# Kernel tuning notes

Hardware: AMD Instinct MI355X
Metric: run time of the kernel (lower is better)

Reference implementation:

```python
import jax, jax.numpy as jnp
import numpy as np

N = 50000   # nodes
E = 800000  # edges
IN, H, C = 256, 128, 4


def _gcn_norm(edge_index, n):
    """Add self-loops and compute symmetric GCN normalization per edge."""
    loops = jnp.arange(n, dtype=edge_index.dtype)
    src = jnp.concatenate([edge_index[0], loops])
    dst = jnp.concatenate([edge_index[1], loops])
    deg = jax.ops.segment_sum(jnp.ones_like(dst, dtype=jnp.float32), dst,
                              num_segments=n)
    dinv = jnp.where(deg > 0, jax.lax.rsqrt(deg), 0.0)
    norm = dinv[src] * dinv[dst]  # [E+N]
    return src, dst, norm


def _gcn_conv(h, src, dst, norm, W, b, n):
    h = h @ W                              # [N, out]
    msg = h[src] * norm[:, None]           # gather + scale, [E+N, out]
    agg = jax.ops.segment_sum(msg, dst, num_segments=n)
    return agg + b


def setup_inputs() -> dict:
    key = jax.random.key(0)
    ks = jax.random.split(key, 5)
    x = jax.random.normal(ks[0], (N, IN), dtype=jnp.float32)
    edge_index = jax.random.randint(ks[1], (2, E), 0, N, dtype=jnp.int32)
    W1 = jax.random.normal(ks[2], (IN, H), dtype=jnp.float32) * (1.0 / np.sqrt(IN))
    b1 = jnp.zeros((H,), dtype=jnp.float32)
    W2 = jax.random.normal(ks[3], (H, C), dtype=jnp.float32) * (1.0 / np.sqrt(H))
    b2 = jnp.zeros((C,), dtype=jnp.float32)
    return {"x": x, "edge_index": edge_index, "W1": W1, "b1": b1,
            "W2": W2, "b2": b2}


def reference(x, edge_index, W1, b1, W2, b2):
    n = x.shape[0]
    src, dst, norm = _gcn_norm(edge_index, n)
    h = jax.nn.relu(_gcn_conv(x, src, dst, norm, W1, b1, n))
    out = _gcn_conv(h, src, dst, norm, W2, b2, n)
    return out
```

## Files before the change

### kernel.cpp

```cpp
#include <hip/hip_runtime.h>
#include <stdint.h>

typedef __attribute__((ext_vector_type(8))) short short8;
typedef __attribute__((ext_vector_type(4))) float f32x4;
typedef __attribute__((ext_vector_type(8))) uint16_t u16x8;

#define EPB 8192
#define BKT_SHIFT 8

static __device__ __forceinline__ uint16_t f_to_bf16(float f) {
  uint32_t u = __float_as_uint(f);
  uint32_t rounding = 0x7fffu + ((u >> 16) & 1u);
  return (uint16_t)((u + rounding) >> 16);
}

__global__ __launch_bounds__(256) void k_bcount(const int* __restrict__ ei, int E,
                                                int* __restrict__ bcnt) {
  __shared__ int hist[256];
  int tid = threadIdx.x;
  hist[tid] = 0;
  __syncthreads();
  int base = blockIdx.x * EPB;
  int nT = min(EPB, E - base);
  for (int i = tid; i < nT; i += 256)
    atomicAdd(&hist[ei[E + base + i] >> BKT_SHIFT], 1);
  __syncthreads();
  int v = hist[tid];
  if (v) atomicAdd(&bcnt[tid], v);
}

__global__ __launch_bounds__(256) void k_bscan(const int* __restrict__ bcnt, int nbkt,
                                               int* __restrict__ bbase,
                                               int* __restrict__ wbase,
                                               int* __restrict__ row_ptr, int n, int E) {
  __shared__ int ws[4];
  int tid = threadIdx.x, lane = tid & 63, wid = tid >> 6;
  int v = (tid < nbkt) ? bcnt[tid] : 0;
  int s = v;
  #pragma unroll
  for (int off = 1; off < 64; off <<= 1) {
    int t2 = __shfl_up(s, off);
    if (lane >= off) s += t2;
  }
  if (lane == 63) ws[wid] = s;
  __syncthreads();
  int add = 0;
  #pragma unroll
  for (int w = 0; w < 4; ++w)
    if (w < wid) add += ws[w];
  int excl = add + s - v;
  if (tid <= nbkt) bbase[tid] = excl;
  if (tid < nbkt) wbase[tid] = excl;
  if (tid == 0) row_ptr[n] = E;
}

__global__ __launch_bounds__(256) void k_bscatter(const int* __restrict__ ei, int E,
                                                  int* __restrict__ wbase,
                                                  uint32_t* __restrict__ coo) {
  __shared__ uint32_t pk[EPB], pko[EPB];
  __shared__ uint8_t bk[EPB], bko[EPB];
  __shared__ int hist[256], hscan[256], gbase[256], cur[256];
  __shared__ int ws[4];
  int tid = threadIdx.x;
  hist[tid] = 0;
  cur[tid] = 0;
  __syncthreads();
  int base = blockIdx.x * EPB;
  int nT = min(EPB, E - base);
  for (int i = tid; i < nT; i += 256) {
    int s = ei[base + i];
    int d = ei[E + base + i];
    int b = d >> BKT_SHIFT;
    pk[i] = ((uint32_t)(d & ((1 << BKT_SHIFT) - 1)) << 16) | (uint32_t)s;
    bk[i] = (uint8_t)b;
    atomicAdd(&hist[b], 1);
  }
  __syncthreads();
  {
    int lane = tid & 63, wid = tid >> 6;
    int v = hist[tid], s = v;
    #pragma unroll
    for (int off = 1; off < 64; off <<= 1) {
      int t2 = __shfl_up(s, off);
      if (lane >= off) s += t2;
    }
    if (lane == 63) ws[wid] = s;
    __syncthreads();
    int add = 0;
    #pragma unroll
    for (int w = 0; w < 4; ++w)
      if (w < wid) add += ws[w];
    hscan[tid] = add + s - v;
    if (v) gbase[tid] = atomicAdd(&wbase[tid], v);
  }
  __syncthreads();
  for (int i = tid; i < nT; i += 256) {
    int b = bk[i];
    int p = hscan[b] + atomicAdd(&cur[b], 1);
    pko[p] = pk[i];
    bko[p] = (uint8_t)b;
  }
  __syncthreads();
  for (int i = tid; i < nT; i += 256) {
    int b = bko[i];
    coo[gbase[b] + (i - hscan[b])] = pko[i];
  }
}

__global__ __launch_bounds__(256) void k_bcsr(const uint32_t* __restrict__ coo,
                                              const int* __restrict__ bbase,
                                              int* __restrict__ row_ptr,
                                              float* __restrict__ dinv,
                                              int* __restrict__ col, int n) {
  __shared__ int hist[256], lscan[256], cur[256];
  __shared__ int ws[4];
  int tid = threadIdx.x, bkt = blockIdx.x;
  int base = bbase[bkt];
  int cnt = bbase[bkt + 1] - base;
  hist[tid] = 0;
  cur[tid] = 0;
  __syncthreads();
  for (int i = tid; i < cnt; i += 256)
    atomicAdd(&hist[coo[base + i] >> 16], 1);
  __syncthreads();
  {
    int lane = tid & 63, wid = tid >> 6;
    int v = hist[tid], s = v;
    #pragma unroll
    for (int off = 1; off < 64; off <<= 1) {
      int t2 = __shfl_up(s, off);
      if (lane >= off) s += t2;
    }
    if (lane == 63) ws[wid] = s;
    __syncthreads();
    int add = 0;
    #pragma unroll
    for (int w = 0; w < 4; ++w)
      if (w < wid) add += ws[w];
    lscan[tid] = add + s - v;
  }
  __syncthreads();
  int v = (bkt << BKT_SHIFT) + tid;
  if (v < n) {
    row_ptr[v] = base + lscan[tid];
    dinv[v] = rsqrtf((float)(hist[tid] + 1));
  }
  for (int i = tid; i < cnt; i += 256) {
    uint32_t p = coo[base + i];
    int local = p >> 16;
    int pos = lscan[local] + atomicAdd(&cur[local], 1);
    col[base + pos] = (int)(p & 0xffffu);
  }
}

__global__ void k_transpose_w1(const float* __restrict__ W1,
                               uint16_t* __restrict__ W1t) {
  int i = blockIdx.x * blockDim.x + threadIdx.x;
  int k = i >> 7, nn = i & 127;
  W1t[nn * 256 + k] = f_to_bf16(W1[i]);
}

__global__ __launch_bounds__(256) void k_gemm1(const float* __restrict__ x,
                                               const uint16_t* __restrict__ W1t,
                                               const float* __restrict__ dinv,
                                               uint16_t* __restrict__ g, int n) {
  constexpr int LDB = 264;
  __shared__ uint16_t bT[128 * LDB];
  int tid = threadIdx.x, lane = tid & 63, wid = tid >> 6;
  int brow = blockIdx.x * 128;

  {
    int row = tid >> 1, half = tid & 1;
    const u16x8* src = (const u16x8*)(W1t + row * 256 + half * 128);
    u16x8* dst = (u16x8*)(bT + row * LDB + half * 128);
    #pragma unroll
    for (int j = 0; j < 16; ++j) dst[j] = src[j];
  }
  __syncthreads();

  f32x4 acc[2][8];
  #pragma unroll
  for (int i = 0; i < 2; ++i)
    #pragma unroll
    for (int j = 0; j < 8; ++j) acc[i][j] = (f32x4)0.0f;

  int r0 = brow + wid * 32 + (lane & 15);
  int r1 = r0 + 16;
  const float* xr0 = x + (size_t)r0 * 256 + (lane >> 4) * 8;
  const float* xr1 = x + (size_t)r1 * 256 + (lane >> 4) * 8;
  bool ok0 = r0 < n, ok1 = r1 < n;

  #pragma unroll 2
  for (int ks = 0; ks < 8; ++ks) {
    f32x4 a0a = ok0 ? *(const f32x4*)(xr0 + ks * 32) : (f32x4)0.0f;
    f32x4 a0b = ok0 ? *(const f32x4*)(xr0 + ks * 32 + 4) : (f32x4)0.0f;
    f32x4 a1a = ok1 ? *(const f32x4*)(xr1 + ks * 32) : (f32x4)0.0f;
    f32x4 a1b = ok1 ? *(const f32x4*)(xr1 + ks * 32 + 4) : (f32x4)0.0f;
    short8 af0, af1;
    #pragma unroll
    for (int j = 0; j < 4; ++j) {
      af0[j] = (short)f_to_bf16(a0a[j]);
      af0[4 + j] = (short)f_to_bf16(a0b[j]);
      af1[j] = (short)f_to_bf16(a1a[j]);
      af1[4 + j] = (short)f_to_bf16(a1b[j]);
    }
    #pragma unroll
    for (int nt = 0; nt < 8; ++nt) {
      short8 bfr = *(const short8*)&bT[(nt * 16 + (lane & 15)) * LDB + ks * 32 + (lane >> 4) * 8];
      acc[0][nt] = __builtin_amdgcn_mfma_f32_16x16x32_bf16(af0, bfr, acc[0][nt], 0, 0, 0);
      acc[1][nt] = __builtin_amdgcn_mfma_f32_16x16x32_bf16(af1, bfr, acc[1][nt], 0, 0, 0);
    }
  }
  #pragma unroll
  for (int rf = 0; rf < 2; ++rf) {
    #pragma unroll
    for (int r = 0; r < 4; ++r) {
      int orow = brow + wid * 32 + rf * 16 + (lane >> 4) * 4 + r;
      if (orow < n) {
        float dv = dinv[orow];
        #pragma unroll
        for (int nt = 0; nt < 8; ++nt) {
          g[(size_t)orow * 128 + nt * 16 + (lane & 15)] = f_to_bf16(acc[rf][nt][r] * dv);
        }
      }
    }
  }
}

__global__ __launch_bounds__(256) void k_agg1(const uint16_t* __restrict__ g,
                                              const int* __restrict__ row_ptr,
                                              const int* __restrict__ col,
                                              const float* __restrict__ dinv,
                                              const float* __restrict__ b1,
                                              const float* __restrict__ W2,
                                              float* __restrict__ g2, int n) {
  int lane = threadIdx.x & 63, wid = threadIdx.x >> 6;
  int v = blockIdx.x * 4 + wid;
  if (v >= n) return;
  const uint32_t* gw = (const uint32_t*)g;
  uint32_t u = gw[(size_t)v * 64 + lane];
  float s0 = __uint_as_float(u << 16);
  float s1 = __uint_as_float(u & 0xffff0000u);
  int beg = row_ptr[v], end = row_ptr[v + 1];
  for (int base = beg; base < end; base += 64) {
    int idx = base + lane;
    int cv = (idx < end) ? col[idx] : v;
    int m = min(64, end - base);
    int nb = (m + 15) >> 4;
    for (int t = 0; t < nb; ++t) {
      int bb = t * 16;
      uint32_t r[16];
      #pragma unroll
      for (int j = 0; j < 16; ++j) {
        int uu = __shfl(cv, bb + j);
        r[j] = gw[(size_t)uu * 64 + lane];
      }
      int mm = m - bb;
      #pragma unroll
      for (int j = 0; j < 16; ++j) {
        if (j < mm) {
          s0 += __uint_as_float(r[j] << 16);
          s1 += __uint_as_float(r[j] & 0xffff0000u);
        }
      }
    }
  }
  float dv = dinv[v];
  float h0 = fmaxf(dv * s0 + b1[2 * lane], 0.0f);
  float h1 = fmaxf(dv * s1 + b1[2 * lane + 1], 0.0f);
  f32x4 w0 = *(const f32x4*)&W2[lane * 8];
  f32x4 w1 = *(const f32x4*)&W2[lane * 8 + 4];
  float p[4];
  #pragma unroll
  for (int c = 0; c < 4; ++c) p[c] = h0 * w0[c] + h1 * w1[c];
  #pragma unroll
  for (int off = 1; off < 64; off <<= 1) {
    #pragma unroll
    for (int c = 0; c < 4; ++c) p[c] += __shfl_xor(p[c], off);
  }
  if (lane == 0) {
    f32x4 o = {dv * p[0], dv * p[1], dv * p[2], dv * p[3]};
    *(f32x4*)&g2[(size_t)v * 4] = o;
  }
}

__global__ void k_agg2(const float* __restrict__ g2, const int* __restrict__ row_ptr,
                       const int* __restrict__ col, const float* __restrict__ dinv,
                       const float* __restrict__ b2, float* __restrict__ out,
                       int n) {
  int v = blockIdx.x * blockDim.x + threadIdx.x;
  if (v >= n) return;
  const f32x4* g4 = (const f32x4*)g2;
  f32x4 a = g4[v];
  int j = row_ptr[v], end = row_ptr[v + 1];
  for (; j + 8 <= end; j += 8) {
    int u[8];
    #pragma unroll
    for (int q = 0; q < 8; ++q) u[q] = col[j + q];
    f32x4 r[8];
    #pragma unroll
    for (int q = 0; q < 8; ++q) r[q] = g4[u[q]];
    a += ((r[0] + r[1]) + (r[2] + r[3])) + ((r[4] + r[5]) + (r[6] + r[7]));
  }
  for (; j < end; ++j) a += g4[col[j]];
  float dv = dinv[v];
  f32x4 o;
  #pragma unroll
  for (int c = 0; c < 4; ++c) o[c] = dv * a[c] + b2[c];
  *(f32x4*)&out[(size_t)v * 4] = o;
}

extern "C" void kernel_launch(void* const* d_in, const int* in_sizes, int n_in,
                              void* d_out, int out_size, void* d_ws, size_t ws_size,
                              hipStream_t stream) {
  const float* x  = (const float*)d_in[0];
  const int* ei   = (const int*)d_in[1];
  const float* W1 = (const float*)d_in[2];
  const float* b1 = (const float*)d_in[3];
  const float* W2 = (const float*)d_in[4];
  const float* b2 = (const float*)d_in[5];
  float* out = (float*)d_out;
  int n = in_sizes[0] / 256;
  int E = in_sizes[1] / 2;
  int nbkt = (n + 255) >> BKT_SHIFT;

  char* ws = (char*)d_ws;
  size_t off = 0;
  auto alloc = [&](size_t bytes) -> void* {
    void* p = (void*)(ws + off);
    off += (bytes + 255) & ~(size_t)255;
    return p;
  };
  int* bcnt     = (int*)alloc((size_t)nbkt * 4);
  int* bbase    = (int*)alloc((size_t)(nbkt + 1) * 4);
  int* wbase    = (int*)alloc((size_t)nbkt * 4);
  uint32_t* coo = (uint32_t*)alloc((size_t)E * 4);
  int* row_ptr  = (int*)alloc((size_t)(n + 1) * 4);
  int* colA     = (int*)alloc((size_t)E * 4);
  float* dinv   = (float*)alloc((size_t)n * 4);
  uint16_t* W1t = (uint16_t*)alloc((size_t)256 * 128 * 2);
  uint16_t* g   = (uint16_t*)alloc((size_t)n * 128 * 2);
  float* g2     = (float*)alloc((size_t)n * 4 * 4);

  int ebk = (E + EPB - 1) / EPB;
  hipMemsetAsync(bcnt, 0, (size_t)nbkt * 4, stream);
  k_bcount<<<dim3(ebk), dim3(256), 0, stream>>>(ei, E, bcnt);
  k_bscan<<<dim3(1), dim3(256), 0, stream>>>(bcnt, nbkt, bbase, wbase, row_ptr, n, E);
  k_bscatter<<<dim3(ebk), dim3(256), 0, stream>>>(ei, E, wbase, coo);
  k_bcsr<<<dim3(nbkt), dim3(256), 0, stream>>>(coo, bbase, row_ptr, dinv, colA, n);
  k_transpose_w1<<<dim3(128), dim3(256), 0, stream>>>(W1, W1t);
  k_gemm1<<<dim3((n + 127) / 128), dim3(256), 0, stream>>>(x, W1t, dinv, g, n);
  k_agg1<<<dim3((n + 3) / 4), dim3(256), 0, stream>>>(g, row_ptr, colA, dinv, b1, W2, g2, n);
  k_agg2<<<dim3((n + 255) / 256), dim3(256), 0, stream>>>(g2, row_ptr, colA, dinv, b2, out, n);
}
```

Measured before the change: 192.9 us.

## Fold bucket scan and W1 prep into neighbouring kernels, prelayout W1 fragments

Result: faster. 186.4 us (-3.4%).

```diff
diff --git a/kernel.cpp b/kernel.cpp
--- a/kernel.cpp
+++ b/kernel.cpp
@@ -1,11 +1,12 @@
 #include <hip/hip_runtime.h>
+#include <hip/hip_bf16.h>
 #include <stdint.h>
 
 typedef __attribute__((ext_vector_type(8))) short short8;
 typedef __attribute__((ext_vector_type(4))) float f32x4;
 typedef __attribute__((ext_vector_type(8))) uint16_t u16x8;
 
-#define EPB 8192
+#define EPB 2048
 #define BKT_SHIFT 8
 
 static __device__ __forceinline__ uint16_t f_to_bf16(float f) {
@@ -13,11 +14,46 @@
   uint32_t rounding = 0x7fffu + ((u >> 16) & 1u);
   return (uint16_t)((u + rounding) >> 16);
 }
-
-__global__ __launch_bounds__(256) void k_bcount(const int* __restrict__ ei, int E,
-                                                int* __restrict__ bcnt) {
+static __device__ __forceinline__ uint32_t pk2_bf16(float a, float b) {
+  float2 f2; f2.x = a; f2.y = b;
+  __hip_bfloat162 h = __float22bfloat162_rn(f2);
+  return *reinterpret_cast<uint32_t*>(&h);
+}
+
+static __device__ __forceinline__ int excl_scan256(int v, int* ws, int tid) {
+  int lane = tid & 63, wid = tid >> 6;
+  int s = v;
+  #pragma unroll
+  for (int off = 1; off < 64; off <<= 1) {
+    int t2 = __shfl_up(s, off);
+    if (lane >= off) s += t2;
+  }
+  if (lane == 63) ws[wid] = s;
+  __syncthreads();
+  int add = 0;
+  #pragma unroll
+  for (int w = 0; w < 4; ++w)
+    if (w < wid) add += ws[w];
+  return add + s - v;
+}
+
+__global__ __launch_bounds__(256) void k_bcount_w1(const int* __restrict__ ei, int E,
+                                                   int ebk, int* __restrict__ bcnt,
+                                                   const float* __restrict__ W1,
+                                                   uint16_t* __restrict__ w1f) {
+  int tid = threadIdx.x;
+  if (blockIdx.x >= ebk) {
+    int s = (blockIdx.x - ebk) * 256 + tid;
+    int lane = s & 63, ks = (s >> 6) & 7, nt = s >> 9;
+    int n = nt * 16 + (lane & 15);
+    int kb = ks * 32 + (lane >> 4) * 8;
+    u16x8 o;
+    #pragma unroll
+    for (int j = 0; j < 8; ++j) o[j] = f_to_bf16(W1[(kb + j) * 128 + n]);
+    *(u16x8*)&w1f[(size_t)s * 8] = o;
+    return;
+  }
   __shared__ int hist[256];
-  int tid = threadIdx.x;
   hist[tid] = 0;
   __syncthreads();
   int base = blockIdx.x * EPB;
@@ -29,33 +65,9 @@
   if (v) atomicAdd(&bcnt[tid], v);
 }
 
-__global__ __launch_bounds__(256) void k_bscan(const int* __restrict__ bcnt, int nbkt,
-                                               int* __restrict__ bbase,
-                                               int* __restrict__ wbase,
-                                               int* __restrict__ row_ptr, int n, int E) {
-  __shared__ int ws[4];
-  int tid = threadIdx.x, lane = tid & 63, wid = tid >> 6;
-  int v = (tid < nbkt) ? bcnt[tid] : 0;
-  int s = v;
-  #pragma unroll
-  for (int off = 1; off < 64; off <<= 1) {
-    int t2 = __shfl_up(s, off);
-    if (lane >= off) s += t2;
-  }
-  if (lane == 63) ws[wid] = s;
-  __syncthreads();
-  int add = 0;
-  #pragma unroll
-  for (int w = 0; w < 4; ++w)
-    if (w < wid) add += ws[w];
-  int excl = add + s - v;
-  if (tid <= nbkt) bbase[tid] = excl;
-  if (tid < nbkt) wbase[tid] = excl;
-  if (tid == 0) row_ptr[n] = E;
-}
-
 __global__ __launch_bounds__(256) void k_bscatter(const int* __restrict__ ei, int E,
-                                                  int* __restrict__ wbase,
+                                                  const int* __restrict__ bcnt, int nbkt,
+                                                  int* __restrict__ relcur,
                                                   uint32_t* __restrict__ coo) {
   __shared__ uint32_t pk[EPB], pko[EPB];
   __shared__ uint8_t bk[EPB], bko[EPB];
@@ -76,23 +88,12 @@
     atomicAdd(&hist[b], 1);
   }
   __syncthreads();
-  {
-    int lane = tid & 63, wid = tid >> 6;
-    int v = hist[tid], s = v;
-    #pragma unroll
-    for (int off = 1; off < 64; off <<= 1) {
-      int t2 = __shfl_up(s, off);
-      if (lane >= off) s += t2;
-    }
-    if (lane == 63) ws[wid] = s;
-    __syncthreads();
-    int add = 0;
-    #pragma unroll
-    for (int w = 0; w < 4; ++w)
-      if (w < wid) add += ws[w];
-    hscan[tid] = add + s - v;
-    if (v) gbase[tid] = atomicAdd(&wbase[tid], v);
-  }
+  int myexcl = excl_scan256((tid < nbkt) ? bcnt[tid] : 0, ws, tid);
+  __syncthreads();
+  int v = hist[tid];
+  int hexcl = excl_scan256(v, ws, tid);
+  hscan[tid] = hexcl;
+  if (v) gbase[tid] = myexcl + atomicAdd(&relcur[tid], v);
   __syncthreads();
   for (int i = tid; i < nT; i += 256) {
     int b = bk[i];
@@ -108,43 +109,33 @@
 }
 
 __global__ __launch_bounds__(256) void k_bcsr(const uint32_t* __restrict__ coo,
-                                              const int* __restrict__ bbase,
-                                              int* __restrict__ row_ptr,
+                                              const int* __restrict__ bcnt, int nbkt,
+                                              int E, int* __restrict__ row_ptr,
                                               float* __restrict__ dinv,
                                               int* __restrict__ col, int n) {
   __shared__ int hist[256], lscan[256], cur[256];
   __shared__ int ws[4];
+  __shared__ int base_s;
   int tid = threadIdx.x, bkt = blockIdx.x;
-  int base = bbase[bkt];
-  int cnt = bbase[bkt + 1] - base;
   hist[tid] = 0;
   cur[tid] = 0;
-  __syncthreads();
+  int myexcl = excl_scan256((tid < nbkt) ? bcnt[tid] : 0, ws, tid);
+  if (tid == bkt) base_s = myexcl;
+  __syncthreads();
+  int base = base_s;
+  int cnt = bcnt[bkt];
   for (int i = tid; i < cnt; i += 256)
     atomicAdd(&hist[coo[base + i] >> 16], 1);
   __syncthreads();
-  {
-    int lane = tid & 63, wid = tid >> 6;
-    int v = hist[tid], s = v;
-    #pragma unroll
-    for (int off = 1; off < 64; off <<= 1) {
-      int t2 = __shfl_up(s, off);
-      if (lane >= off) s += t2;
-    }
-    if (lane == 63) ws[wid] = s;
-    __syncthreads();
-    int add = 0;
-    #pragma unroll
-    for (int w = 0; w < 4; ++w)
-      if (w < wid) add += ws[w];
-    lscan[tid] = add + s - v;
-  }
+  int lexcl = excl_scan256(hist[tid], ws, tid);
+  lscan[tid] = lexcl;
   __syncthreads();
   int v = (bkt << BKT_SHIFT) + tid;
   if (v < n) {
-    row_ptr[v] = base + lscan[tid];
+    row_ptr[v] = base + lexcl;
     dinv[v] = rsqrtf((float)(hist[tid] + 1));
   }
+  if (bkt == 0 && tid == 0) row_ptr[n] = E;
   for (int i = tid; i < cnt; i += 256) {
     uint32_t p = coo[base + i];
     int local = p >> 16;
@@ -153,28 +144,19 @@
   }
 }
 
-__global__ void k_transpose_w1(const float* __restrict__ W1,
-                               uint16_t* __restrict__ W1t) {
-  int i = blockIdx.x * blockDim.x + threadIdx.x;
-  int k = i >> 7, nn = i & 127;
-  W1t[nn * 256 + k] = f_to_bf16(W1[i]);
-}
-
 __global__ __launch_bounds__(256) void k_gemm1(const float* __restrict__ x,
-                                               const uint16_t* __restrict__ W1t,
+                                               const uint16_t* __restrict__ w1f,
                                                const float* __restrict__ dinv,
                                                uint16_t* __restrict__ g, int n) {
-  constexpr int LDB = 264;
-  __shared__ uint16_t bT[128 * LDB];
+  __shared__ uint16_t bF[32768];
   int tid = threadIdx.x, lane = tid & 63, wid = tid >> 6;
   int brow = blockIdx.x * 128;
 
   {
-    int row = tid >> 1, half = tid & 1;
-    const u16x8* src = (const u16x8*)(W1t + row * 256 + half * 128);
-    u16x8* dst = (u16x8*)(bT + row * LDB + half * 128);
-    #pragma unroll
-    for (int j = 0; j < 16; ++j) dst[j] = src[j];
+    const u16x8* src = (const u16x8*)w1f;
+    u16x8* dst = (u16x8*)bF;
+    #pragma unroll
+    for (int j = 0; j < 16; ++j) dst[tid + j * 256] = src[tid + j * 256];
   }
   __syncthreads();
 
@@ -196,19 +178,20 @@
     f32x4 a0b = ok0 ? *(const f32x4*)(xr0 + ks * 32 + 4) : (f32x4)0.0f;
     f32x4 a1a = ok1 ? *(const f32x4*)(xr1 + ks * 32) : (f32x4)0.0f;
     f32x4 a1b = ok1 ? *(const f32x4*)(xr1 + ks * 32 + 4) : (f32x4)0.0f;
-    short8 af0, af1;
-    #pragma unroll
-    for (int j = 0; j < 4; ++j) {
-      af0[j] = (short)f_to_bf16(a0a[j]);
-      af0[4 + j] = (short)f_to_bf16(a0b[j]);
-      af1[j] = (short)f_to_bf16(a1a[j]);
-      af1[4 + j] = (short)f_to_bf16(a1b[j]);
-    }
+    union { short8 s; uint32_t u[4]; } af0, af1;
+    af0.u[0] = pk2_bf16(a0a[0], a0a[1]);
+    af0.u[1] = pk2_bf16(a0a[2], a0a[3]);
+    af0.u[2] = pk2_bf16(a0b[0], a0b[1]);
+    af0.u[3] = pk2_bf16(a0b[2], a0b[3]);
+    af1.u[0] = pk2_bf16(a1a[0], a1a[1]);
+    af1.u[1] = pk2_bf16(a1a[2], a1a[3]);
+    af1.u[2] = pk2_bf16(a1b[0], a1b[1]);
+    af1.u[3] = pk2_bf16(a1b[2], a1b[3]);
     #pragma unroll
     for (int nt = 0; nt < 8; ++nt) {
-      short8 bfr = *(const short8*)&bT[(nt * 16 + (lane & 15)) * LDB + ks * 32 + (lane >> 4) * 8];
-      acc[0][nt] = __builtin_amdgcn_mfma_f32_16x16x32_bf16(af0, bfr, acc[0][nt], 0, 0, 0);
-      acc[1][nt] = __builtin_amdgcn_mfma_f32_16x16x32_bf16(af1, bfr, acc[1][nt], 0, 0, 0);
+      short8 bfr = *(const short8*)&bF[((nt * 8 + ks) * 64 + lane) * 8];
+      acc[0][nt] = __builtin_amdgcn_mfma_f32_16x16x32_bf16(af0.s, bfr, acc[0][nt], 0, 0, 0);
+      acc[1][nt] = __builtin_amdgcn_mfma_f32_16x16x32_bf16(af1.s, bfr, acc[1][nt], 0, 0, 0);
     }
   }
   #pragma unroll
@@ -331,25 +314,22 @@
     off += (bytes + 255) & ~(size_t)255;
     return p;
   };
-  int* bcnt     = (int*)alloc((size_t)nbkt * 4);
-  int* bbase    = (int*)alloc((size_t)(nbkt + 1) * 4);
-  int* wbase    = (int*)alloc((size_t)nbkt * 4);
+  int* bcnt     = (int*)alloc((size_t)nbkt * 2 * 4);
+  int* relcur   = bcnt + nbkt;
   uint32_t* coo = (uint32_t*)alloc((size_t)E * 4);
   int* row_ptr  = (int*)alloc((size_t)(n + 1) * 4);
   int* colA     = (int*)alloc((size_t)E * 4);
   float* dinv   = (float*)alloc((size_t)n * 4);
-  uint16_t* W1t = (uint16_t*)alloc((size_t)256 * 128 * 2);
+  uint16_t* w1f = (uint16_t*)alloc((size_t)256 * 128 * 2);
   uint16_t* g   = (uint16_t*)alloc((size_t)n * 128 * 2);
   float* g2     = (float*)alloc((size_t)n * 4 * 4);
 
   int ebk = (E + EPB - 1) / EPB;
-  hipMemsetAsync(bcnt, 0, (size_t)nbkt * 4, stream);
-  k_bcount<<<dim3(ebk), dim3(256), 0, stream>>>(ei, E, bcnt);
-  k_bscan<<<dim3(1), dim3(256), 0, stream>>>(bcnt, nbkt, bbase, wbase, row_ptr, n, E);
-  k_bscatter<<<dim3(ebk), dim3(256), 0, stream>>>(ei, E, wbase, coo);
-  k_bcsr<<<dim3(nbkt), dim3(256), 0, stream>>>(coo, bbase, row_ptr, dinv, colA, n);
-  k_transpose_w1<<<dim3(128), dim3(256), 0, stream>>>(W1, W1t);
-  k_gemm1<<<dim3((n + 127) / 128), dim3(256), 0, stream>>>(x, W1t, dinv, g, n);
+  hipMemsetAsync(bcnt, 0, (size_t)nbkt * 2 * 4, stream);
+  k_bcount_w1<<<dim3(ebk + 16), dim3(256), 0, stream>>>(ei, E, ebk, bcnt, W1, w1f);
+  k_bscatter<<<dim3(ebk), dim3(256), 0, stream>>>(ei, E, bcnt, nbkt, relcur, coo);
+  k_bcsr<<<dim3(nbkt), dim3(256), 0, stream>>>(coo, bcnt, nbkt, E, row_ptr, dinv, colA, n);
+  k_gemm1<<<dim3((n + 127) / 128), dim3(256), 0, stream>>>(x, w1f, dinv, g, n);
   k_agg1<<<dim3((n + 3) / 4), dim3(256), 0, stream>>>(g, row_ptr, colA, dinv, b1, W2, g2, n);
   k_agg2<<<dim3((n + 255) / 256), dim3(256), 0, stream>>>(g2, row_ptr, colA, dinv, b2, out, n);
 }
```
